# Kernel tuning notes

Hardware: AMD Instinct MI355X
Metric: run time of the kernel (lower is better)

Reference implementation:

```python
import jax, jax.numpy as jnp
import numpy as np

EPS = 1e-07
B, C, NCON, NCC = 500000, 30, 8, 3
NH = 7  # hidden width


def _coarse_code():
    # [C, NCC] Gaussian bump coarse code, as built in __init__
    sigma = 0.25
    const_1 = 1.0 / (sigma * np.sqrt(6.28))
    ii = jnp.arange(C, dtype=jnp.float32)[:, None] / (C - 1)
    jj = jnp.arange(NCC, dtype=jnp.float32)[None, :] / (NCC - 1)
    return (const_1 * jnp.exp(-0.5 * jnp.square((ii - jj) / sigma))).astype(jnp.float32)


def _mlp(x, W1, b1, Wh, bh, Wo, bo):
    # x: [B, C, n_in]; six 7-unit ReLU layers then linear output (dropout inactive)
    h = jax.nn.relu(jnp.einsum('bci,hi->bch', x, W1) + b1)
    for i in range(Wh.shape[0]):
        h = jax.nn.relu(jnp.einsum('bci,hi->bch', h, Wh[i]) + bh[i])
    return jnp.einsum('bci,oi->bco', h, Wo) + bo


def setup_inputs() -> dict:
    key = jax.random.key(0)
    ks = jax.random.split(key, 16)
    u = lambda k, shape, lo, hi: jax.random.uniform(k, shape, jnp.float32, lo, hi)
    inp = {
        'tau': jax.random.uniform(ks[0], (B, C, NCON), jnp.float32),
        'mu_direct': jax.random.uniform(ks[1], (B, 1), jnp.float32),
        'mu_diffuse': jax.random.uniform(ks[2], (B, 1), jnp.float32),
        # net_direct: n_input = 5 + NCC + 1 = 9
        'Wd1': u(ks[3], (NH, 5 + NCC + 1), -1.0, 1.0),
        'bd1': u(ks[4], (NH,), 0.9, 1.1),
        'Wdh': u(ks[5], (5, NH, NH), -1.0, 1.0),
        'bdh': u(ks[6], (5, NH), 0.9, 1.1),
        'Wdo': u(ks[7], (3, NH), -1.0, 1.0),
        'bdo': u(ks[8], (3,), -0.1, 0.1),
        # net_diffuse: n_input = 5 + NCC = 8
        'Wf1': u(ks[9], (NH, 5 + NCC), -1.0, 1.0),
        'bf1': u(ks[10], (NH,), 0.9, 1.1),
        'Wfh': u(ks[11], (5, NH, NH), -1.0, 1.0),
        'bfh': u(ks[12], (5, NH), 0.9, 1.1),
        'Wfo': u(ks[13], (3, NH), -1.0, 1.0),
        'bfo': u(ks[14], (3,), -0.1, 0.1),
    }
    return inp


def reference(tau, mu_direct, mu_diffuse, Wd1, bd1, Wdh, bdh, Wdo, bdo,
              Wf1, bf1, Wfh, bfh, Wfo, bfo):
    tau_total = jnp.sum(tau, axis=2)                      # [B, C]
    t_direct = jnp.exp(-tau_total / (mu_direct + EPS))    # [B, C]
    t_diffuse = jnp.exp(-tau_total / (mu_diffuse + EPS))  # [B, C]

    mu_d = mu_direct[:, :, None]                          # [B, 1, 1]
    tau_direct = tau / (mu_d + EPS)                       # [B, C, NCON]

    direct_1 = (tau_direct[:, :, 3] + tau_direct[:, :, 4]
                + tau_direct[:, :, 6] + tau_direct[:, :, 7])[:, :, None]
    mu_rep = jnp.broadcast_to(mu_d, (tau.shape[0], C, 1))
    cc = jnp.broadcast_to(_coarse_code()[None], (tau.shape[0], C, NCC))

    direct = jnp.concatenate([tau_direct[:, :, 0:2], tau_direct[:, :, 5:6],
                              tau_direct[:, :, 2:3], direct_1, mu_rep, cc], axis=2)  # [B,C,9]

    diffuse_1 = (tau[:, :, 3] + tau[:, :, 4] + tau[:, :, 6] + tau[:, :, 7])[:, :, None]
    diffuse = jnp.concatenate([tau[:, :, 0:2], tau[:, :, 5:6],
                               tau[:, :, 2:3], diffuse_1, cc], axis=2)  # [B,C,8]

    e_split_direct = jax.nn.softmax(_mlp(direct, Wd1, bd1, Wdh, bdh, Wdo, bdo), axis=-1)
    e_split_diffuse = jax.nn.softmax(_mlp(diffuse, Wf1, bf1, Wfh, bfh, Wfo, bfo), axis=-1)
    return (t_direct, t_diffuse, e_split_direct, e_split_diffuse)
```

## Files before the change

### kernel.cpp

```cpp
#include <hip/hip_runtime.h>


#define B_SZ 500000
#define C_SZ 30
#define BC   (B_SZ * C_SZ)
#define HBC  (BC / 2)
#define EPSF 1e-7f
#define LOG2E 1.4426950408889634f

typedef float f2 __attribute__((ext_vector_type(2)));

enum {
    WD1P  = 0,
    WF1P  = 48,
    WDHP  = 96,
    WFHP  = 376,
    BDHP  = 656,
    BFHP  = 696,
    WDOP  = 736,
    BDOP  = 764,
    WFOP  = 768,
    BFOP  = 796,
    BEFFD = 800,
    BEFFF = 1040,
    WS_FLOATS = 1280
};
#define FLAG_BYTE_OFF 6144

__device__ __forceinline__ float bf2f(unsigned short u) {
    union { unsigned int i; float f; } v;
    v.i = ((unsigned int)u) << 16;
    return v.f;
}

__device__ __forceinline__ unsigned short f2bf(float f) {
    union { float f; unsigned int i; } v;
    v.f = f;
    unsigned int u = v.i;
    unsigned int r = u + 0x7fffu + ((u >> 16) & 1u);
    return (unsigned short)(r >> 16);
}

__device__ __forceinline__ float ex2(float x) {
    float r;
    asm("v_exp_f32 %0, %1" : "=v"(r) : "v"(x));
    return r;
}

__device__ __forceinline__ unsigned int pk_bf16(float lo, float hi) {
    unsigned int r;
    asm("v_cvt_pk_bf16_f32 %0, %1, %2" : "=v"(r) : "v"(lo), "v"(hi));
    return r;
}

__device__ __forceinline__ f2 pkfma(f2 a, f2 b, f2 c) {
#if __has_builtin(__builtin_elementwise_fma)
    return __builtin_elementwise_fma(a, b, c);
#else
    f2 r; r.x = fmaf(a.x, b.x, c.x); r.y = fmaf(a.y, b.y, c.y); return r;
#endif
}

__device__ __forceinline__ f2 pkmax0(f2 a) {
    f2 z = {0.0f, 0.0f};
#if __has_builtin(__builtin_elementwise_max)
    return __builtin_elementwise_max(a, z);
#else
    f2 r; r.x = fmaxf(a.x, 0.f); r.y = fmaxf(a.y, 0.f); return r;
#endif
}

__device__ __forceinline__ f2 bc(f2 v, int hl) {
    return hl ? __builtin_shufflevector(v, v, 1, 1)
              : __builtin_shufflevector(v, v, 0, 0);
}

struct P12 { const void* p[12]; };

__global__ void prep(P12 ptrs, const unsigned int* __restrict__ tau_raw,
                     float* __restrict__ ws, int* __restrict__ flagp)
{
    __shared__ int sflag;
    int tid = threadIdx.x;
    if (tid < 64) {
        unsigned long long m = __ballot((tau_raw[tid] & 0x8000u) != 0u);
        if (tid == 0) { sflag = (m != 0ull) ? 1 : 0; *flagp = sflag; }
    }
    __syncthreads();
    const int f32m = sflag;

    auto rd = [&](int seg, int idx) -> float {
        if (f32m) return ((const float*)ptrs.p[seg])[idx];
        return bf2f(((const unsigned short*)ptrs.p[seg])[idx]);
    };
    auto ccf = [&](int c, int k) -> float {
        const float C1 = 1.0f / (0.25f * sqrtf(6.28f));
        float ii = (float)c * (1.0f / 29.0f);
        float jj = (float)k * 0.5f;
        float d = (ii - jj) * 4.0f;
        return C1 * expf(-0.5f * d * d);
    };

    for (int i = tid; i < 48; i += 256) {
        int ii = i >> 3, p = (i >> 1) & 3, hl = i & 1, j = 2 * p + hl;
        ws[WD1P + i] = (j < 7) ? rd(0, j * 9 + ii) : 0.f;
    }
    for (int i = tid; i < 48; i += 256) {
        int ii = i >> 3, p = (i >> 1) & 3, hl = i & 1, j = 2 * p + hl;
        ws[WF1P + i] = (j < 7 && ii < 5) ? rd(6, j * 8 + ii) : 0.f;
    }
    for (int i = tid; i < 280; i += 256) {
        int l = i / 56, r = i % 56;
        int ii = r >> 3, p = (r >> 1) & 3, hl = r & 1, j = 2 * p + hl;
        ws[WDHP + i] = (j < 7) ? rd(2, l * 49 + j * 7 + ii) : 0.f;
        ws[WFHP + i] = (j < 7) ? rd(8, l * 49 + j * 7 + ii) : 0.f;
    }
    for (int i = tid; i < 40; i += 256) {
        int l = i / 8, p = (i >> 1) & 3, hl = i & 1, j = 2 * p + hl;
        ws[BDHP + i] = (j < 7) ? rd(3, l * 7 + j) : 0.f;
        ws[BFHP + i] = (j < 7) ? rd(9, l * 7 + j) : 0.f;
    }
    for (int i = tid; i < 28; i += 256) {
        int ii = i >> 2, p = (i >> 1) & 1, hl = i & 1, k = 2 * p + hl;
        ws[WDOP + i] = (k < 3) ? rd(4, k * 7 + ii) * LOG2E : 0.f;
        ws[WFOP + i] = (k < 3) ? rd(10, k * 7 + ii) * LOG2E : 0.f;
    }
    for (int i = tid; i < 4; i += 256) {
        ws[BDOP + i] = (i < 3) ? rd(5, i) * LOG2E : 0.f;
        ws[BFOP + i] = (i < 3) ? rd(11, i) * LOG2E : 0.f;
    }
    for (int i = tid; i < 240; i += 256) {
        int c = i / 8, j = i % 8; float v = 0.f;
        if (j < 7) v = rd(1, j) + rd(0, j * 9 + 6) * ccf(c, 0)
                               + rd(0, j * 9 + 7) * ccf(c, 1)
                               + rd(0, j * 9 + 8) * ccf(c, 2);
        ws[BEFFD + i] = v;
    }
    for (int i = tid; i < 240; i += 256) {
        int c = i / 8, j = i % 8; float v = 0.f;
        if (j < 7) v = rd(7, j) + rd(6, j * 8 + 5) * ccf(c, 0)
                               + rd(6, j * 8 + 6) * ccf(c, 1)
                               + rd(6, j * 8 + 7) * ccf(c, 2);
        ws[BEFFF + i] = v;
    }
}

__global__ __launch_bounds__(256, 4) void scatter_main(
    const void* __restrict__ tau_p,
    const void* __restrict__ mu_dir_p,
    const void* __restrict__ mu_dif_p,
    const float* __restrict__ ws,
    const int* __restrict__ flag,
    void* __restrict__ out_p)
{
    __shared__ unsigned short sm[2][2048];

    int tid = threadIdx.x;
    int eb0 = blockIdx.x * 256;
    int e0 = eb0 + tid;
    bool act = (e0 < HBC);
    int eL = act ? e0 : (HBC - 1);
    int b0 = eL / C_SZ;
    int c  = eL - b0 * C_SZ;
    int b1 = b0 + (HBC / C_SZ);
    bool tail = (eb0 + 256 > HBC);

    int is_f32 = *flag;

    float T[2][8], MUD[2], MUF[2];
    if (is_f32) {
        const float4* tf = (const float4*)tau_p;
#pragma unroll
        for (int h = 0; h < 2; ++h) {
            int ee = eL + h * HBC;
            float4 a = tf[2 * ee], bq = tf[2 * ee + 1];
            T[h][0] = a.x;  T[h][1] = a.y;  T[h][2] = a.z;  T[h][3] = a.w;
            T[h][4] = bq.x; T[h][5] = bq.y; T[h][6] = bq.z; T[h][7] = bq.w;
        }
        MUD[0] = ((const float*)mu_dir_p)[b0];
        MUD[1] = ((const float*)mu_dir_p)[b1];
        MUF[0] = ((const float*)mu_dif_p)[b0];
        MUF[1] = ((const float*)mu_dif_p)[b1];
    } else {
        const uint4* tu = (const uint4*)tau_p;
#pragma unroll
        for (int h = 0; h < 2; ++h) {
            uint4 t = tu[eL + h * HBC];
            T[h][0] = bf2f((unsigned short)(t.x & 0xffffu));
            T[h][1] = bf2f((unsigned short)(t.x >> 16));
            T[h][2] = bf2f((unsigned short)(t.y & 0xffffu));
            T[h][3] = bf2f((unsigned short)(t.y >> 16));
            T[h][4] = bf2f((unsigned short)(t.z & 0xffffu));
            T[h][5] = bf2f((unsigned short)(t.z >> 16));
            T[h][6] = bf2f((unsigned short)(t.w & 0xffffu));
            T[h][7] = bf2f((unsigned short)(t.w >> 16));
        }
        MUD[0] = bf2f(((const unsigned short*)mu_dir_p)[b0]);
        MUD[1] = bf2f(((const unsigned short*)mu_dir_p)[b1]);
        MUF[0] = bf2f(((const unsigned short*)mu_dif_p)[b0]);
        MUF[1] = bf2f(((const unsigned short*)mu_dif_p)[b1]);
    }

    f2 bed[4], bef[4];
    {
        const float4* q = (const float4*)(ws + BEFFD) + 2 * c;
        float4 qa = q[0], qb = q[1];
        bed[0] = f2{qa.x, qa.y}; bed[1] = f2{qa.z, qa.w};
        bed[2] = f2{qb.x, qb.y}; bed[3] = f2{qb.z, qb.w};
        const float4* r = (const float4*)(ws + BEFFF) + 2 * c;
        float4 ra = r[0], rb = r[1];
        bef[0] = f2{ra.x, ra.y}; bef[1] = f2{ra.z, ra.w};
        bef[2] = f2{rb.x, rb.y}; bef[3] = f2{rb.z, rb.w};
    }

    float tdir[2], tdif[2];
    f2 xd[2][3], xf[2][3];
#pragma unroll
    for (int h = 0; h < 2; ++h) {
        float rcp_d = __builtin_amdgcn_rcpf(MUD[h] + EPSF);
        float rcp_f = __builtin_amdgcn_rcpf(MUF[h] + EPSF);
        float tt = ((T[h][0] + T[h][1]) + (T[h][2] + T[h][3]))
                 + ((T[h][4] + T[h][5]) + (T[h][6] + T[h][7]));
        float ttl = tt * LOG2E;
        tdir[h] = ex2(-ttl * rcp_d);
        tdif[h] = ex2(-ttl * rcp_f);
        float s1 = (T[h][3] + T[h][4]) + (T[h][6] + T[h][7]);
        xd[h][0] = f2{T[h][0] * rcp_d, T[h][1] * rcp_d};
        xd[h][1] = f2{T[h][5] * rcp_d, T[h][2] * rcp_d};
        xd[h][2] = f2{s1 * rcp_d, MUD[h]};
        xf[h][0] = f2{T[h][0], T[h][1]};
        xf[h][1] = f2{T[h][5], T[h][2]};
        xf[h][2] = f2{s1, 0.0f};
    }

    f2 hD[2][4], hF[2][4];
#pragma unroll
    for (int p = 0; p < 4; ++p) {
        hD[0][p] = bed[p]; hD[1][p] = bed[p];
        hF[0][p] = bef[p]; hF[1][p] = bef[p];
    }
    {
        const f2* w1d = (const f2*)(ws + WD1P);
        const f2* w1f = (const f2*)(ws + WF1P);
#pragma unroll
        for (int i = 0; i < 6; ++i) {
            f2 a0 = bc(xd[0][i >> 1], i & 1), a1 = bc(xd[1][i >> 1], i & 1);
            f2 b0v = bc(xf[0][i >> 1], i & 1), b1v = bc(xf[1][i >> 1], i & 1);
#pragma unroll
            for (int p = 0; p < 4; ++p) {
                f2 wd = w1d[i * 4 + p], wf = w1f[i * 4 + p];
                hD[0][p] = pkfma(a0, wd, hD[0][p]);
                hD[1][p] = pkfma(a1, wd, hD[1][p]);
                hF[0][p] = pkfma(b0v, wf, hF[0][p]);
                hF[1][p] = pkfma(b1v, wf, hF[1][p]);
            }
        }
#pragma unroll
        for (int p = 0; p < 4; ++p) {
            hD[0][p] = pkmax0(hD[0][p]); hD[1][p] = pkmax0(hD[1][p]);
            hF[0][p] = pkmax0(hF[0][p]); hF[1][p] = pkmax0(hF[1][p]);
        }
    }
    {
        const f2* whd = (const f2*)(ws + WDHP);
        const f2* whf = (const f2*)(ws + WFHP);
        const f2* bhd = (const f2*)(ws + BDHP);
        const f2* bhf = (const f2*)(ws + BFHP);
#pragma unroll
        for (int l = 0; l < 5; ++l) {
            f2 nD[2][4], nF[2][4];
#pragma unroll
            for (int p = 0; p < 4; ++p) {
                f2 bd = bhd[l * 4 + p], bfv = bhf[l * 4 + p];
                nD[0][p] = bd;  nD[1][p] = bd;
                nF[0][p] = bfv; nF[1][p] = bfv;
            }
#pragma unroll
            for (int i = 0; i < 7; ++i) {
                f2 a0 = bc(hD[0][i >> 1], i & 1), a1 = bc(hD[1][i >> 1], i & 1);
                f2 c0 = bc(hF[0][i >> 1], i & 1), c1 = bc(hF[1][i >> 1], i & 1);
#pragma unroll
                for (int p = 0; p < 4; ++p) {
                    f2 wd = whd[(l * 7 + i) * 4 + p], wf = whf[(l * 7 + i) * 4 + p];
                    nD[0][p] = pkfma(a0, wd, nD[0][p]);
                    nD[1][p] = pkfma(a1, wd, nD[1][p]);
                    nF[0][p] = pkfma(c0, wf, nF[0][p]);
                    nF[1][p] = pkfma(c1, wf, nF[1][p]);
                }
            }
#pragma unroll
            for (int p = 0; p < 4; ++p) {
                hD[0][p] = pkmax0(nD[0][p]); hD[1][p] = pkmax0(nD[1][p]);
                hF[0][p] = pkmax0(nF[0][p]); hF[1][p] = pkmax0(nF[1][p]);
            }
        }
    }
    float od[2][3], of_[2][3];
    {
        const f2* wod = (const f2*)(ws + WDOP);
        const f2* wof = (const f2*)(ws + WFOP);
        const f2* bod = (const f2*)(ws + BDOP);
        const f2* bof = (const f2*)(ws + BFOP);
        f2 oDa[2] = {bod[0], bod[0]}, oDb[2] = {bod[1], bod[1]};
        f2 oFa[2] = {bof[0], bof[0]}, oFb[2] = {bof[1], bof[1]};
#pragma unroll
        for (int i = 0; i < 7; ++i) {
            f2 w0 = wod[i * 2 + 0], w1 = wod[i * 2 + 1];
            f2 v0 = wof[i * 2 + 0], v1 = wof[i * 2 + 1];
#pragma unroll
            for (int h = 0; h < 2; ++h) {
                f2 ad = bc(hD[h][i >> 1], i & 1);
                f2 af = bc(hF[h][i >> 1], i & 1);
                oDa[h] = pkfma(ad, w0, oDa[h]);
                oDb[h] = pkfma(ad, w1, oDb[h]);
                oFa[h] = pkfma(af, v0, oFa[h]);
                oFb[h] = pkfma(af, v1, oFb[h]);
            }
        }
#pragma unroll
        for (int h = 0; h < 2; ++h) {
            od[h][0] = oDa[h].x; od[h][1] = oDa[h].y; od[h][2] = oDb[h].x;
            of_[h][0] = oFa[h].x; of_[h][1] = oFa[h].y; of_[h][2] = oFb[h].x;
        }
    }

    float D0[2], D1[2], D2[2], F0[2], F1[2], F2[2];
#pragma unroll
    for (int h = 0; h < 2; ++h) {
        float md = fmaxf(fmaxf(od[h][0], od[h][1]), od[h][2]);
        float d0 = ex2(od[h][0] - md), d1 = ex2(od[h][1] - md), d2 = ex2(od[h][2] - md);
        float rdd = __builtin_amdgcn_rcpf(d0 + d1 + d2);
        D0[h] = d0 * rdd; D1[h] = d1 * rdd; D2[h] = d2 * rdd;
        float mf = fmaxf(fmaxf(of_[h][0], of_[h][1]), of_[h][2]);
        float f0 = ex2(of_[h][0] - mf), f1 = ex2(of_[h][1] - mf), f2v = ex2(of_[h][2] - mf);
        float rff = __builtin_amdgcn_rcpf(f0 + f1 + f2v);
        F0[h] = f0 * rff; F1[h] = f1 * rff; F2[h] = f2v * rff;
    }

    if (!is_f32 && !tail) {
#pragma unroll
        for (int h = 0; h < 2; ++h) {
            unsigned int P1 = pk_bf16(tdir[h], tdif[h]);
            unsigned int P2 = pk_bf16(D0[h], D1[h]);
            unsigned int P3 = pk_bf16(D2[h], F0[h]);
            unsigned int P4 = pk_bf16(F1[h], F2[h]);
            sm[h][tid]       = (unsigned short)P1;
            sm[h][256 + tid] = (unsigned short)(P1 >> 16);
            int db = 512 + 3 * tid;
            sm[h][db + 0] = (unsigned short)P2;
            sm[h][db + 1] = (unsigned short)(P2 >> 16);
            sm[h][db + 2] = (unsigned short)P3;
            int fb = 1280 + 3 * tid;
            sm[h][fb + 0] = (unsigned short)(P3 >> 16);
            sm[h][fb + 1] = (unsigned short)P4;
            sm[h][fb + 2] = (unsigned short)(P4 >> 16);
        }
        __syncthreads();
#pragma unroll
        for (int h = 0; h < 2; ++h) {
            uint4 v = ((const uint4*)sm[h])[tid];
            unsigned int E = (h ? (unsigned int)HBC : 0u) + (unsigned int)eb0;
            unsigned int goff;
            if (tid < 32)        goff = 2u * E + 16u * tid;
            else if (tid < 64)   goff = 2u * ((unsigned int)BC + E) + 16u * (tid - 32);
            else if (tid < 160)  goff = 4u * (unsigned int)BC + 6u * E + 16u * (tid - 64);
            else                 goff = 10u * (unsigned int)BC + 6u * E + 16u * (tid - 160);
            *(uint4*)((char*)out_p + goff) = v;
        }
    } else if (!is_f32) {
        if (act) {
            unsigned short* out = (unsigned short*)out_p;
#pragma unroll
            for (int h = 0; h < 2; ++h) {
                int e = e0 + h * HBC;
                int odb = 2 * BC + 3 * e;
                int ofb = 5 * BC + 3 * e;
                out[e]       = f2bf(tdir[h]);
                out[BC + e]  = f2bf(tdif[h]);
                out[odb + 0] = f2bf(D0[h]);
                out[odb + 1] = f2bf(D1[h]);
                out[odb + 2] = f2bf(D2[h]);
                out[ofb + 0] = f2bf(F0[h]);
                out[ofb + 1] = f2bf(F1[h]);
                out[ofb + 2] = f2bf(F2[h]);
            }
        }
    } else {
        if (act) {
            float* out = (float*)out_p;
#pragma unroll
            for (int h = 0; h < 2; ++h) {
                int e = e0 + h * HBC;
                int odb = 2 * BC + 3 * e;
                int ofb = 5 * BC + 3 * e;
                out[e] = tdir[h];
                out[BC + e] = tdif[h];
                out[odb + 0] = D0[h]; out[odb + 1] = D1[h]; out[odb + 2] = D2[h];
                out[ofb + 0] = F0[h]; out[ofb + 1] = F1[h]; out[ofb + 2] = F2[h];
            }
        }
    }
}

extern "C" void kernel_launch(void* const* d_in, const int* in_sizes, int n_in,
                              void* d_out, int out_size, void* d_ws, size_t ws_size,
                              hipStream_t stream) {
    float* ws = (float*)d_ws;
    int* flag = (int*)((char*)d_ws + FLAG_BYTE_OFF);

    P12 p;
    for (int i = 0; i < 12; ++i) p.p[i] = d_in[3 + i];
    prep<<<1, 256, 0, stream>>>(p, (const unsigned int*)d_in[0], ws, flag);

    int nblk = (HBC + 255) / 256;
    scatter_main<<<nblk, 256, 0, stream>>>(
        d_in[0], d_in[1], d_in[2], ws, flag, d_out);
}
```

Before: 839.1 us.

## Use fp16 dot2 for diffuse MLP and trim padded 7th lane in packed FMA

The padded 8-wide packed-FMA MLP becomes three packed pairs plus one scalar lane, removing the wasted eighth hidden unit. When inputs are bf16, the diffuse MLP uses v_dot2 fp16 instructions on half-packed activations and weights, which roughly halves its VALU work. Both rely on a new weight layout built in the prep kernel. The cost is lower intermediate precision in the diffuse network, from fp16 rounding with round-toward-zero conversion, and more code paths.

```diff
diff --git a/kernel.cpp b/kernel.cpp
--- a/kernel.cpp
+++ b/kernel.cpp
@@ -8,22 +8,40 @@
 #define EPSF 1e-7f
 #define LOG2E 1.4426950408889634f
 
+#if __has_builtin(__builtin_amdgcn_fdot2)
+#define HAVE_FDOT2 1
+#else
+#define HAVE_FDOT2 0
+#endif
+
 typedef float f2 __attribute__((ext_vector_type(2)));
+typedef __fp16 h2 __attribute__((ext_vector_type(2)));
 
 enum {
     WD1P  = 0,
-    WF1P  = 48,
-    WDHP  = 96,
-    WFHP  = 376,
-    BDHP  = 656,
-    BFHP  = 696,
-    WDOP  = 736,
-    BDOP  = 764,
-    WFOP  = 768,
-    BFOP  = 796,
-    BEFFD = 800,
-    BEFFF = 1040,
-    WS_FLOATS = 1280
+    WD1S  = 36,
+    WDHP  = 42,
+    WDHS  = 252,
+    BDHP  = 288,
+    BDHS  = 318,
+    WDOP  = 324,
+    BDOP  = 352,
+    BEFFD = 360,
+    BEFFF = 600,
+    BFH   = 840,
+    BFOF  = 876,
+    VF16  = 880,
+    WFH16 = 908,
+    WFO16 = 1048,
+    VF1P  = 1060,
+    VF1S  = 1096,
+    VFHP  = 1102,
+    VFHS  = 1312,
+    BFHP  = 1348,
+    BFHS  = 1378,
+    VFOP  = 1384,
+    BFOP  = 1412,
+    WS_FLOATS = 1416
 };
 #define FLAG_BYTE_OFF 6144
 
@@ -73,6 +91,85 @@
 __device__ __forceinline__ f2 bc(f2 v, int hl) {
     return hl ? __builtin_shufflevector(v, v, 1, 1)
               : __builtin_shufflevector(v, v, 0, 0);
+}
+
+__device__ __forceinline__ h2 uash2(unsigned int u) {
+    union { unsigned int u; h2 h; } v; v.u = u; return v.h;
+}
+
+template <int W1P, int W1S, int WHP, int WHS, int BHP, int BHS, int WOP, int BOP>
+__device__ __forceinline__ void mlp_ps2(const float* __restrict__ ws,
+                                        const f2 x[2][3], const f2 be[4],
+                                        float o[2][3]) {
+    const f2* w1 = (const f2*)(ws + W1P);
+    f2 hP[2][3]; float hS[2];
+#pragma unroll
+    for (int h = 0; h < 2; ++h) {
+        hP[h][0] = be[0]; hP[h][1] = be[1]; hP[h][2] = be[2];
+        hS[h] = be[3].x;
+    }
+#pragma unroll
+    for (int i = 0; i < 6; ++i) {
+        f2 xb0 = bc(x[0][i >> 1], i & 1), xb1 = bc(x[1][i >> 1], i & 1);
+        float wsc = ws[W1S + i];
+#pragma unroll
+        for (int p = 0; p < 3; ++p) {
+            f2 w = w1[i * 3 + p];
+            hP[0][p] = pkfma(xb0, w, hP[0][p]);
+            hP[1][p] = pkfma(xb1, w, hP[1][p]);
+        }
+        hS[0] = fmaf(xb0.x, wsc, hS[0]);
+        hS[1] = fmaf(xb1.x, wsc, hS[1]);
+    }
+#pragma unroll
+    for (int h = 0; h < 2; ++h) {
+        hP[h][0] = pkmax0(hP[h][0]); hP[h][1] = pkmax0(hP[h][1]);
+        hP[h][2] = pkmax0(hP[h][2]); hS[h] = fmaxf(hS[h], 0.f);
+    }
+    const f2* wh = (const f2*)(ws + WHP);
+    const f2* bh = (const f2*)(ws + BHP);
+#pragma unroll
+    for (int l = 0; l < 5; ++l) {
+        f2 nP[2][3]; float nS[2];
+#pragma unroll
+        for (int p = 0; p < 3; ++p) { f2 b = bh[l * 3 + p]; nP[0][p] = b; nP[1][p] = b; }
+        nS[0] = ws[BHS + l]; nS[1] = nS[0];
+#pragma unroll
+        for (int i = 0; i < 7; ++i) {
+            f2 xb0 = (i < 6) ? bc(hP[0][i >> 1], i & 1) : f2{hS[0], hS[0]};
+            f2 xb1 = (i < 6) ? bc(hP[1][i >> 1], i & 1) : f2{hS[1], hS[1]};
+            float wsc = ws[WHS + l * 7 + i];
+#pragma unroll
+            for (int p = 0; p < 3; ++p) {
+                f2 w = wh[(l * 7 + i) * 3 + p];
+                nP[0][p] = pkfma(xb0, w, nP[0][p]);
+                nP[1][p] = pkfma(xb1, w, nP[1][p]);
+            }
+            nS[0] = fmaf(xb0.x, wsc, nS[0]);
+            nS[1] = fmaf(xb1.x, wsc, nS[1]);
+        }
+#pragma unroll
+        for (int h = 0; h < 2; ++h) {
+            hP[h][0] = pkmax0(nP[h][0]); hP[h][1] = pkmax0(nP[h][1]);
+            hP[h][2] = pkmax0(nP[h][2]); hS[h] = fmaxf(nS[h], 0.f);
+        }
+    }
+    const f2* wo = (const f2*)(ws + WOP);
+    const f2* bo = (const f2*)(ws + BOP);
+    f2 oA[2] = {bo[0], bo[0]}, oB[2] = {bo[1], bo[1]};
+#pragma unroll
+    for (int i = 0; i < 7; ++i) {
+#pragma unroll
+        for (int h = 0; h < 2; ++h) {
+            f2 xb = (i < 6) ? bc(hP[h][i >> 1], i & 1) : f2{hS[h], hS[h]};
+            oA[h] = pkfma(xb, wo[i * 2 + 0], oA[h]);
+            oB[h] = pkfma(xb, wo[i * 2 + 1], oB[h]);
+        }
+    }
+#pragma unroll
+    for (int h = 0; h < 2; ++h) {
+        o[h][0] = oA[h].x; o[h][1] = oA[h].y; o[h][2] = oB[h].x;
+    }
 }
 
 struct P12 { const void* p[12]; };
@@ -100,35 +197,39 @@
         float d = (ii - jj) * 4.0f;
         return C1 * expf(-0.5f * d * d);
     };
-
-    for (int i = tid; i < 48; i += 256) {
-        int ii = i >> 3, p = (i >> 1) & 3, hl = i & 1, j = 2 * p + hl;
-        ws[WD1P + i] = (j < 7) ? rd(0, j * 9 + ii) : 0.f;
-    }
-    for (int i = tid; i < 48; i += 256) {
-        int ii = i >> 3, p = (i >> 1) & 3, hl = i & 1, j = 2 * p + hl;
-        ws[WF1P + i] = (j < 7 && ii < 5) ? rd(6, j * 8 + ii) : 0.f;
-    }
-    for (int i = tid; i < 280; i += 256) {
-        int l = i / 56, r = i % 56;
-        int ii = r >> 3, p = (r >> 1) & 3, hl = r & 1, j = 2 * p + hl;
-        ws[WDHP + i] = (j < 7) ? rd(2, l * 49 + j * 7 + ii) : 0.f;
-        ws[WFHP + i] = (j < 7) ? rd(8, l * 49 + j * 7 + ii) : 0.f;
-    }
-    for (int i = tid; i < 40; i += 256) {
-        int l = i / 8, p = (i >> 1) & 3, hl = i & 1, j = 2 * p + hl;
-        ws[BDHP + i] = (j < 7) ? rd(3, l * 7 + j) : 0.f;
-        ws[BFHP + i] = (j < 7) ? rd(9, l * 7 + j) : 0.f;
-    }
+    auto pk = [&](float a, float b) -> unsigned int {
+        union { h2 h; unsigned int u; } v;
+        v.h.x = (__fp16)a; v.h.y = (__fp16)b;
+        return v.u;
+    };
+    unsigned int* wsu = (unsigned int*)ws;
+
+    for (int i = tid; i < 36; i += 256) {
+        int ii = i / 6, r = i % 6, p = r >> 1, hl = r & 1, j = 2 * p + hl;
+        ws[WD1P + i] = rd(0, j * 9 + ii);
+    }
+    for (int i = tid; i < 6; i += 256) ws[WD1S + i] = rd(0, 6 * 9 + i);
+    for (int i = tid; i < 210; i += 256) {
+        int l = i / 42, r = i % 42, ii = r / 6, rr = r % 6;
+        int p = rr >> 1, hl = rr & 1, j = 2 * p + hl;
+        ws[WDHP + i] = rd(2, l * 49 + j * 7 + ii);
+    }
+    for (int i = tid; i < 35; i += 256) {
+        int l = i / 7, ii = i % 7;
+        ws[WDHS + i] = rd(2, l * 49 + 6 * 7 + ii);
+    }
+    for (int i = tid; i < 30; i += 256) {
+        int l = i / 6, r = i % 6, p = r >> 1, hl = r & 1, j = 2 * p + hl;
+        ws[BDHP + i] = rd(3, l * 7 + j);
+    }
+    for (int i = tid; i < 5; i += 256) ws[BDHS + i] = rd(3, i * 7 + 6);
     for (int i = tid; i < 28; i += 256) {
         int ii = i >> 2, p = (i >> 1) & 1, hl = i & 1, k = 2 * p + hl;
         ws[WDOP + i] = (k < 3) ? rd(4, k * 7 + ii) * LOG2E : 0.f;
-        ws[WFOP + i] = (k < 3) ? rd(10, k * 7 + ii) * LOG2E : 0.f;
-    }
-    for (int i = tid; i < 4; i += 256) {
+    }
+    for (int i = tid; i < 4; i += 256)
         ws[BDOP + i] = (i < 3) ? rd(5, i) * LOG2E : 0.f;
-        ws[BFOP + i] = (i < 3) ? rd(11, i) * LOG2E : 0.f;
-    }
+
     for (int i = tid; i < 240; i += 256) {
         int c = i / 8, j = i % 8; float v = 0.f;
         if (j < 7) v = rd(1, j) + rd(0, j * 9 + 6) * ccf(c, 0)
@@ -143,6 +244,55 @@
                                + rd(6, j * 8 + 7) * ccf(c, 2);
         ws[BEFFF + i] = v;
     }
+
+    for (int i = tid; i < 35; i += 256) ws[BFH + i] = rd(9, i);
+    for (int i = tid; i < 3; i += 256) ws[BFOF + i] = rd(11, i) * LOG2E;
+    for (int i = tid; i < 28; i += 256) {
+        int j = i / 4, q = i % 4;
+        const int cols[8] = {0, 1, 3, 4, 4, 2, 4, 4};
+        wsu[VF16 + i] = pk(rd(6, j * 8 + cols[2 * q]), rd(6, j * 8 + cols[2 * q + 1]));
+    }
+    for (int i = tid; i < 140; i += 256) {
+        int lj = i / 4, q = i % 4;
+        float lo, hi;
+        if (q < 3) { lo = rd(8, lj * 7 + 2 * q); hi = rd(8, lj * 7 + 2 * q + 1); }
+        else       { lo = rd(8, lj * 7 + 6);     hi = 0.f; }
+        wsu[WFH16 + i] = pk(lo, hi);
+    }
+    for (int i = tid; i < 12; i += 256) {
+        int k = i / 4, q = i % 4;
+        float lo, hi;
+        if (q < 3) { lo = rd(10, k * 7 + 2 * q) * LOG2E; hi = rd(10, k * 7 + 2 * q + 1) * LOG2E; }
+        else       { lo = rd(10, k * 7 + 6) * LOG2E;     hi = 0.f; }
+        wsu[WFO16 + i] = pk(lo, hi);
+    }
+
+    for (int i = tid; i < 36; i += 256) {
+        int ii = i / 6, r = i % 6, p = r >> 1, hl = r & 1, j = 2 * p + hl;
+        ws[VF1P + i] = (ii < 5) ? rd(6, j * 8 + ii) : 0.f;
+    }
+    for (int i = tid; i < 6; i += 256)
+        ws[VF1S + i] = (i < 5) ? rd(6, 6 * 8 + i) : 0.f;
+    for (int i = tid; i < 210; i += 256) {
+        int l = i / 42, r = i % 42, ii = r / 6, rr = r % 6;
+        int p = rr >> 1, hl = rr & 1, j = 2 * p + hl;
+        ws[VFHP + i] = rd(8, l * 49 + j * 7 + ii);
+    }
+    for (int i = tid; i < 35; i += 256) {
+        int l = i / 7, ii = i % 7;
+        ws[VFHS + i] = rd(8, l * 49 + 6 * 7 + ii);
+    }
+    for (int i = tid; i < 30; i += 256) {
+        int l = i / 6, r = i % 6, p = r >> 1, hl = r & 1, j = 2 * p + hl;
+        ws[BFHP + i] = rd(9, l * 7 + j);
+    }
+    for (int i = tid; i < 5; i += 256) ws[BFHS + i] = rd(9, i * 7 + 6);
+    for (int i = tid; i < 28; i += 256) {
+        int ii = i >> 2, p = (i >> 1) & 1, hl = i & 1, k = 2 * p + hl;
+        ws[VFOP + i] = (k < 3) ? rd(10, k * 7 + ii) * LOG2E : 0.f;
+    }
+    for (int i = tid; i < 4; i += 256)
+        ws[BFOP + i] = (i < 3) ? rd(11, i) * LOG2E : 0.f;
 }
 
 __global__ __launch_bounds__(256, 4) void scatter_main(
@@ -213,8 +363,8 @@
         bef[2] = f2{rb.x, rb.y}; bef[3] = f2{rb.z, rb.w};
     }
 
-    float tdir[2], tdif[2];
-    f2 xd[2][3], xf[2][3];
+    float tdir[2], tdif[2], s1v[2];
+    f2 xd[2][3];
 #pragma unroll
     for (int h = 0; h < 2; ++h) {
         float rcp_d = __builtin_amdgcn_rcpf(MUD[h] + EPSF);
@@ -224,104 +374,94 @@
         float ttl = tt * LOG2E;
         tdir[h] = ex2(-ttl * rcp_d);
         tdif[h] = ex2(-ttl * rcp_f);
-        float s1 = (T[h][3] + T[h][4]) + (T[h][6] + T[h][7]);
+        s1v[h] = (T[h][3] + T[h][4]) + (T[h][6] + T[h][7]);
         xd[h][0] = f2{T[h][0] * rcp_d, T[h][1] * rcp_d};
         xd[h][1] = f2{T[h][5] * rcp_d, T[h][2] * rcp_d};
-        xd[h][2] = f2{s1 * rcp_d, MUD[h]};
-        xf[h][0] = f2{T[h][0], T[h][1]};
-        xf[h][1] = f2{T[h][5], T[h][2]};
-        xf[h][2] = f2{s1, 0.0f};
-    }
-
-    f2 hD[2][4], hF[2][4];
-#pragma unroll
-    for (int p = 0; p < 4; ++p) {
-        hD[0][p] = bed[p]; hD[1][p] = bed[p];
-        hF[0][p] = bef[p]; hF[1][p] = bef[p];
-    }
+        xd[h][2] = f2{s1v[h] * rcp_d, MUD[h]};
+    }
+
+    float od[2][3];
+    mlp_ps2<WD1P, WD1S, WDHP, WDHS, BDHP, BDHS, WDOP, BDOP>(ws, xd, bed, od);
+
+    float of_[2][3];
+#if HAVE_FDOT2
+    if (!is_f32) {
+        const unsigned int* wsu = (const unsigned int*)ws;
+        h2 xq[2][4];
+#pragma unroll
+        for (int h = 0; h < 2; ++h) {
+            xq[h][0] = __builtin_amdgcn_cvt_pkrtz(T[h][0], T[h][1]);
+            xq[h][1] = __builtin_amdgcn_cvt_pkrtz(T[h][2], T[h][3]);
+            xq[h][2] = __builtin_amdgcn_cvt_pkrtz(T[h][4], T[h][5]);
+            xq[h][3] = __builtin_amdgcn_cvt_pkrtz(T[h][6], T[h][7]);
+        }
+        float hf[2][7];
+#pragma unroll
+        for (int j = 0; j < 7; ++j) {
+            float b = (j < 6) ? ((j & 1) ? bef[j >> 1].y : bef[j >> 1].x) : bef[3].x;
+            float a0 = b, a1 = b;
+#pragma unroll
+            for (int q = 0; q < 4; ++q) {
+                h2 w = uash2(wsu[VF16 + j * 4 + q]);
+                a0 = __builtin_amdgcn_fdot2(xq[0][q], w, a0, false);
+                a1 = __builtin_amdgcn_fdot2(xq[1][q], w, a1, false);
+            }
+            hf[0][j] = fmaxf(a0, 0.f); hf[1][j] = fmaxf(a1, 0.f);
+        }
+#pragma unroll
+        for (int l = 0; l < 5; ++l) {
+            h2 hp[2][4];
+#pragma unroll
+            for (int h = 0; h < 2; ++h) {
+                hp[h][0] = __builtin_amdgcn_cvt_pkrtz(hf[h][0], hf[h][1]);
+                hp[h][1] = __builtin_amdgcn_cvt_pkrtz(hf[h][2], hf[h][3]);
+                hp[h][2] = __builtin_amdgcn_cvt_pkrtz(hf[h][4], hf[h][5]);
+                hp[h][3] = __builtin_amdgcn_cvt_pkrtz(hf[h][6], 0.f);
+            }
+#pragma unroll
+            for (int j = 0; j < 7; ++j) {
+                float b = ws[BFH + l * 7 + j];
+                float a0 = b, a1 = b;
+#pragma unroll
+                for (int q = 0; q < 4; ++q) {
+                    h2 w = uash2(wsu[WFH16 + (l * 7 + j) * 4 + q]);
+                    a0 = __builtin_amdgcn_fdot2(hp[0][q], w, a0, false);
+                    a1 = __builtin_amdgcn_fdot2(hp[1][q], w, a1, false);
+                }
+                hf[0][j] = fmaxf(a0, 0.f); hf[1][j] = fmaxf(a1, 0.f);
+            }
+        }
+        h2 op[2][4];
+#pragma unroll
+        for (int h = 0; h < 2; ++h) {
+            op[h][0] = __builtin_amdgcn_cvt_pkrtz(hf[h][0], hf[h][1]);
+            op[h][1] = __builtin_amdgcn_cvt_pkrtz(hf[h][2], hf[h][3]);
+            op[h][2] = __builtin_amdgcn_cvt_pkrtz(hf[h][4], hf[h][5]);
+            op[h][3] = __builtin_amdgcn_cvt_pkrtz(hf[h][6], 0.f);
+        }
+#pragma unroll
+        for (int k = 0; k < 3; ++k) {
+            float b = ws[BFOF + k];
+            float a0 = b, a1 = b;
+#pragma unroll
+            for (int q = 0; q < 4; ++q) {
+                h2 w = uash2(wsu[WFO16 + k * 4 + q]);
+                a0 = __builtin_amdgcn_fdot2(op[0][q], w, a0, false);
+                a1 = __builtin_amdgcn_fdot2(op[1][q], w, a1, false);
+            }
+            of_[0][k] = a0; of_[1][k] = a1;
+        }
+    } else
+#endif
     {
-        const f2* w1d = (const f2*)(ws + WD1P);
-        const f2* w1f = (const f2*)(ws + WF1P);
-#pragma unroll
-        for (int i = 0; i < 6; ++i) {
-            f2 a0 = bc(xd[0][i >> 1], i & 1), a1 = bc(xd[1][i >> 1], i & 1);
-            f2 b0v = bc(xf[0][i >> 1], i & 1), b1v = bc(xf[1][i >> 1], i & 1);
-#pragma unroll
-            for (int p = 0; p < 4; ++p) {
-                f2 wd = w1d[i * 4 + p], wf = w1f[i * 4 + p];
-                hD[0][p] = pkfma(a0, wd, hD[0][p]);
-                hD[1][p] = pkfma(a1, wd, hD[1][p]);
-                hF[0][p] = pkfma(b0v, wf, hF[0][p]);
-                hF[1][p] = pkfma(b1v, wf, hF[1][p]);
-            }
-        }
-#pragma unroll
-        for (int p = 0; p < 4; ++p) {
-            hD[0][p] = pkmax0(hD[0][p]); hD[1][p] = pkmax0(hD[1][p]);
-            hF[0][p] = pkmax0(hF[0][p]); hF[1][p] = pkmax0(hF[1][p]);
-        }
-    }
-    {
-        const f2* whd = (const f2*)(ws + WDHP);
-        const f2* whf = (const f2*)(ws + WFHP);
-        const f2* bhd = (const f2*)(ws + BDHP);
-        const f2* bhf = (const f2*)(ws + BFHP);
-#pragma unroll
-        for (int l = 0; l < 5; ++l) {
-            f2 nD[2][4], nF[2][4];
-#pragma unroll
-            for (int p = 0; p < 4; ++p) {
-                f2 bd = bhd[l * 4 + p], bfv = bhf[l * 4 + p];
-                nD[0][p] = bd;  nD[1][p] = bd;
-                nF[0][p] = bfv; nF[1][p] = bfv;
-            }
-#pragma unroll
-            for (int i = 0; i < 7; ++i) {
-                f2 a0 = bc(hD[0][i >> 1], i & 1), a1 = bc(hD[1][i >> 1], i & 1);
-                f2 c0 = bc(hF[0][i >> 1], i & 1), c1 = bc(hF[1][i >> 1], i & 1);
-#pragma unroll
-                for (int p = 0; p < 4; ++p) {
-                    f2 wd = whd[(l * 7 + i) * 4 + p], wf = whf[(l * 7 + i) * 4 + p];
-                    nD[0][p] = pkfma(a0, wd, nD[0][p]);
-                    nD[1][p] = pkfma(a1, wd, nD[1][p]);
-                    nF[0][p] = pkfma(c0, wf, nF[0][p]);
-                    nF[1][p] = pkfma(c1, wf, nF[1][p]);
-                }
-            }
-#pragma unroll
-            for (int p = 0; p < 4; ++p) {
-                hD[0][p] = pkmax0(nD[0][p]); hD[1][p] = pkmax0(nD[1][p]);
-                hF[0][p] = pkmax0(nF[0][p]); hF[1][p] = pkmax0(nF[1][p]);
-            }
-        }
-    }
-    float od[2][3], of_[2][3];
-    {
-        const f2* wod = (const f2*)(ws + WDOP);
-        const f2* wof = (const f2*)(ws + WFOP);
-        const f2* bod = (const f2*)(ws + BDOP);
-        const f2* bof = (const f2*)(ws + BFOP);
-        f2 oDa[2] = {bod[0], bod[0]}, oDb[2] = {bod[1], bod[1]};
-        f2 oFa[2] = {bof[0], bof[0]}, oFb[2] = {bof[1], bof[1]};
-#pragma unroll
-        for (int i = 0; i < 7; ++i) {
-            f2 w0 = wod[i * 2 + 0], w1 = wod[i * 2 + 1];
-            f2 v0 = wof[i * 2 + 0], v1 = wof[i * 2 + 1];
-#pragma unroll
-            for (int h = 0; h < 2; ++h) {
-                f2 ad = bc(hD[h][i >> 1], i & 1);
-                f2 af = bc(hF[h][i >> 1], i & 1);
-                oDa[h] = pkfma(ad, w0, oDa[h]);
-                oDb[h] = pkfma(ad, w1, oDb[h]);
-                oFa[h] = pkfma(af, v0, oFa[h]);
-                oFb[h] = pkfma(af, v1, oFb[h]);
-            }
-        }
-#pragma unroll
-        for (int h = 0; h < 2; ++h) {
-            od[h][0] = oDa[h].x; od[h][1] = oDa[h].y; od[h][2] = oDb[h].x;
-            of_[h][0] = oFa[h].x; of_[h][1] = oFa[h].y; of_[h][2] = oFb[h].x;
-        }
+        f2 xf[2][3];
+#pragma unroll
+        for (int h = 0; h < 2; ++h) {
+            xf[h][0] = f2{T[h][0], T[h][1]};
+            xf[h][1] = f2{T[h][5], T[h][2]};
+            xf[h][2] = f2{s1v[h], 0.0f};
+        }
+        mlp_ps2<VF1P, VF1S, VFHP, VFHS, BFHP, BFHS, VFOP, BFOP>(ws, xf, bef, of_);
     }
 
     float D0[2], D1[2], D2[2], F0[2], F1[2], F2[2];
```

Result: slower. 928.4 us (+10.6%).
